# Performance work log

Hardware: AMD Instinct MI355X
Metric: run time of the kernel (lower is better)

Reference implementation:

```python
import jax, jax.numpy as jnp
import numpy as np

K = 3  # filter_size
PAD = (K - 1) // 2


def setup_inputs() -> dict:
    key = jax.random.key(0)
    k1, k2, k3 = jax.random.split(key, 3)
    B, C, H, Wd = 4, 256, 128, 128
    x = jax.random.normal(k1, (B, C, H, Wd), dtype=jnp.float32)
    # 1x1 conv params: out_channels = C * K^2
    W = jax.random.normal(k2, (C * K * K, C), dtype=jnp.float32) * (1.0 / np.sqrt(C))
    b = jax.random.normal(k3, (C * K * K,), dtype=jnp.float32) * 0.01
    return {"x": x, "W": W, "b": b}


def _extract_patches(x):
    # x: (B,C,H,W) -> (B,C,H,W,K*K), kernel positions row-major (matches F.unfold)
    B, C, H, Wd = x.shape
    xp = jnp.pad(x, ((0, 0), (0, 0), (PAD, PAD), (PAD, PAD)))
    patches = jnp.stack(
        [xp[:, :, i:i + H, j:j + Wd] for i in range(K) for j in range(K)],
        axis=-1,
    )
    return patches


def reference(x, W, b):
    B, C, H, Wd = x.shape
    # 1x1 conv: (B,C,H,W) x (C*K^2, C) -> (B, C*K^2, H, W)
    filters = jnp.einsum('bchw,oc->bohw', x, W) + b[None, :, None, None]
    # view(B, C, K^2, H, W) then permute to (B,C,H,W,K^2)
    filters = filters.reshape(B, C, K * K, H, Wd).transpose(0, 1, 3, 4, 2)
    patches = _extract_patches(x)  # (B,C,H,W,K^2), unfold ordering c-major then pos
    return jnp.sum(patches * filters, axis=-1)  # (B,C,H,W)
```

## Files before the change

### kernel.cpp

```cpp
#include <hip/hip_runtime.h>


typedef __attribute__((ext_vector_type(8))) short bf16x8;
typedef __attribute__((ext_vector_type(4))) float f32x4;

__device__ __forceinline__ unsigned int f2bf(float f) {
    unsigned int u = __float_as_uint(f);
    return (u + 0x7fffu + ((u >> 16) & 1u)) >> 16;
}
__device__ __forceinline__ unsigned int pack2(float a, float b) {
    return f2bf(a) | (f2bf(b) << 16);
}

__global__ __launch_bounds__(256) void wconv_kernel(const float* __restrict__ W,
                                                    unsigned char* __restrict__ Wb) {
    int idx0 = blockIdx.x * 256 + threadIdx.x;
    int o = idx0 >> 5, g = idx0 & 31;
    const float4* src = (const float4*)(W + ((size_t)o << 8) + ((size_t)g << 3));
    float4 v0 = src[0], v1 = src[1];
    uint4 pk;
    pk.x = pack2(v0.x, v0.y); pk.y = pack2(v0.z, v0.w);
    pk.z = pack2(v1.x, v1.y); pk.w = pack2(v1.z, v1.w);
    int kh = g >> 4, g2 = g & 15, s = g2 >> 2, kq = g2 & 3;
    int chunk = o / 144, oc = o - chunk * 144;
    int c_local = oc / 9, p = oc - c_local * 9;
    int q = c_local >> 2, c4 = c_local & 3;
    int idx = c4 * 9 + p;
    int ni = idx >> 2, j = idx & 3, r = (q << 2) + j;
    int jsub = kh * 3 + ni / 3, ni_ = ni % 3;
    size_t dst = (size_t)chunk * 73728 + (size_t)jsub * 12288
               + (size_t)(s * 3 + ni_) * 1024 + (size_t)((kq << 4) + r) * 16;
    *(uint4*)(Wb + dst) = pk;
}


#define SYNC_VM(N) asm volatile("s_waitcnt vmcnt(" #N ") lgkmcnt(0)\n\ts_barrier" ::: "memory")
#define SYNC_LG    asm volatile("s_waitcnt lgkmcnt(0)\n\ts_barrier" ::: "memory")
#define FENCE      asm volatile("" ::: "memory")

#define STAGE(CH, J)                                                            \
    do {                                                                        \
        const unsigned char* bs_ = Wb + (size_t)(CH) * 73728                    \
            + (size_t)(J) * 12288 + wv * 3072 + (lane << 4);                    \
        unsigned char* bd_ = smem + (size_t)(J) * 12288 + wv * 3072;            \
        _Pragma("unroll")                                                       \
        for (int c_ = 0; c_ < 3; ++c_)                                          \
            __builtin_amdgcn_global_load_lds(                                   \
                (const __attribute__((address_space(1))) void*)(bs_ + c_ * 1024), \
                (__attribute__((address_space(3))) void*)(bd_ + c_ * 1024), 16, 0, 0); \
    } while (0)

#define MFMA_SUB(J)                                                             \
    do {                                                                        \
        const int kh_ = (J) / 3, snib_ = ((J) % 3) * 3;                         \
        const unsigned char* bb_ = smem + (size_t)(J) * 12288 + (lane << 4);    \
        _Pragma("unroll")                                                       \
        for (int s_ = 0; s_ < 4; ++s_) {                                        \
            const bf16x8 a0_ = afr[(kh_ << 2) + s_];                            \
            const bf16x8 a1_ = afr[8 + (kh_ << 2) + s_];                        \
            _Pragma("unroll")                                                   \
            for (int ni_ = 0; ni_ < 3; ++ni_) {                                 \
                const bf16x8 bq_ = *(const bf16x8*)(bb_ + ((s_ * 3 + ni_) << 10)); \
                acc[0][snib_ + ni_] = __builtin_amdgcn_mfma_f32_16x16x32_bf16(  \
                    bq_, a0_, acc[0][snib_ + ni_], 0, 0, 0);                    \
                acc[1][snib_ + ni_] = __builtin_amdgcn_mfma_f32_16x16x32_bf16(  \
                    bq_, a1_, acc[1][snib_ + ni_], 0, 0, 0);                    \
            }                                                                   \
        }                                                                       \
    } while (0)

__global__ __launch_bounds__(256, 2) void dfgemm_kernel(
        const unsigned char* __restrict__ Wb, const float* __restrict__ x,
        const float* __restrict__ bias, float* __restrict__ out) {
    __shared__ __align__(16) unsigned char smem[73728];

    const int t = threadIdx.x;
    const int lane = t & 63, wv = t >> 6;
    const int quad = lane >> 4, lrow = lane & 15;

    const int b = blockIdx.x >> 7;
    const int h = blockIdx.x & 127;

    STAGE(0, 0); STAGE(0, 1); STAGE(0, 2);
    STAGE(0, 3); STAGE(0, 4); STAGE(0, 5);

    bf16x8 afr[16];
    {
        const float* xrow = x + ((size_t)b << 22) + (h << 7);
        #pragma unroll
        for (int mi = 0; mi < 2; ++mi) {
            const int w = (wv << 5) + (mi << 4) + lrow;
            #pragma unroll
            for (int gg = 0; gg < 8; ++gg) {
                const float* p = xrow + ((size_t)((gg << 5) + (quad << 3)) << 14) + w;
                float v[8];
                #pragma unroll
                for (int e = 0; e < 8; ++e) v[e] = p[(size_t)e << 14];
                uint4 pk;
                pk.x = pack2(v[0], v[1]); pk.y = pack2(v[2], v[3]);
                pk.z = pack2(v[4], v[5]); pk.w = pack2(v[6], v[7]);
                afr[(mi << 3) + gg] = *(const bf16x8*)&pk;
            }
        }
    }
    SYNC_VM(0);

    #pragma unroll 1
    for (int chunk = 0; chunk < 16; ++chunk) {
        const int c1 = (chunk + 1) & 15;
        f32x4 acc[2][9];
        const f32x4 zero = {0.f, 0.f, 0.f, 0.f};
        #pragma unroll
        for (int mi = 0; mi < 2; ++mi)
            #pragma unroll
            for (int ni = 0; ni < 9; ++ni) acc[mi][ni] = zero;

        SYNC_VM(8);

        MFMA_SUB(0); MFMA_SUB(1); MFMA_SUB(2);
        MFMA_SUB(3); MFMA_SUB(4); MFMA_SUB(5);

        SYNC_LG;

        STAGE(c1, 0); STAGE(c1, 1); STAGE(c1, 2);
        STAGE(c1, 3); STAGE(c1, 4); STAGE(c1, 5);
        FENCE;

        #pragma unroll
        for (int mi = 0; mi < 2; ++mi) {
            const int w = (wv << 5) + (mi << 4) + lrow;
            #pragma unroll
            for (int c4 = 0; c4 < 4; ++c4) {
                const int cg = (chunk << 4) + (quad << 2) + c4;
                const float* bp = bias + cg * 9;
                const float* xc = x + ((size_t)((b << 8) + cg) << 14);
                float sum = 0.f;
                #pragma unroll
                for (int p = 0; p < 9; ++p) {
                    const int idx = c4 * 9 + p;
                    const int ni = idx >> 2, j = idx & 3;
                    const float yv = acc[mi][ni][j];
                    const int hh = h + p / 3 - 1, ww = w + p % 3 - 1;
                    float xv = 0.f;
                    if ((unsigned)hh < 128u && (unsigned)ww < 128u)
                        xv = xc[(hh << 7) + ww];
                    sum += (yv + bp[p]) * xv;
                }
                out[((size_t)((b << 8) + cg) << 14) + (h << 7) + w] = sum;
            }
        }
    }
}

extern "C" void kernel_launch(void* const* d_in, const int* in_sizes, int n_in,
                              void* d_out, int out_size, void* d_ws, size_t ws_size,
                              hipStream_t stream) {
    const float* x    = (const float*)d_in[0];
    const float* W    = (const float*)d_in[1];
    const float* bias = (const float*)d_in[2];
    float* out = (float*)d_out;

    unsigned char* Wb = (unsigned char*)d_ws;

    wconv_kernel<<<288, 256, 0, stream>>>(W, Wb);
    dfgemm_kernel<<<512, 256, 0, stream>>>(Wb, x, bias, out);
}
```

Measured before the change: 204.1 us.

## Split channel chunks across two blocks and ring-buffer weight staging in LDS

Each row is now handled by two blocks that each process half of the 16 channel chunks, which doubles the grid. Weight staging moves from a full 72KB chunk buffer to a 4-slot 48KB ring, and the next sub-tile loads are interleaved with the MFMA on the current one using finer vmcnt waits. The smaller LDS footprint allows 3 blocks per CU. The trade-off is that every block re-reads and re-converts the full input row fragment, so x loads double, and there are more barriers per chunk.

```diff
diff --git a/kernel.cpp b/kernel.cpp
--- a/kernel.cpp
+++ b/kernel.cpp
@@ -35,14 +35,13 @@
 
 
 #define SYNC_VM(N) asm volatile("s_waitcnt vmcnt(" #N ") lgkmcnt(0)\n\ts_barrier" ::: "memory")
-#define SYNC_LG    asm volatile("s_waitcnt lgkmcnt(0)\n\ts_barrier" ::: "memory")
 #define FENCE      asm volatile("" ::: "memory")
 
-#define STAGE(CH, J)                                                            \
+#define STAGE(CH, J, BUF)                                                       \
     do {                                                                        \
         const unsigned char* bs_ = Wb + (size_t)(CH) * 73728                    \
             + (size_t)(J) * 12288 + wv * 3072 + (lane << 4);                    \
-        unsigned char* bd_ = smem + (size_t)(J) * 12288 + wv * 3072;            \
+        unsigned char* bd_ = smem + (size_t)(BUF) * 12288 + wv * 3072;          \
         _Pragma("unroll")                                                       \
         for (int c_ = 0; c_ < 3; ++c_)                                          \
             __builtin_amdgcn_global_load_lds(                                   \
@@ -50,10 +49,10 @@
                 (__attribute__((address_space(3))) void*)(bd_ + c_ * 1024), 16, 0, 0); \
     } while (0)
 
-#define MFMA_SUB(J)                                                             \
+#define MFMA_SUB(J, BUF)                                                        \
     do {                                                                        \
         const int kh_ = (J) / 3, snib_ = ((J) % 3) * 3;                         \
-        const unsigned char* bb_ = smem + (size_t)(J) * 12288 + (lane << 4);    \
+        const unsigned char* bb_ = smem + (size_t)(BUF) * 12288 + (lane << 4);  \
         _Pragma("unroll")                                                       \
         for (int s_ = 0; s_ < 4; ++s_) {                                        \
             const bf16x8 a0_ = afr[(kh_ << 2) + s_];                            \
@@ -69,20 +68,22 @@
         }                                                                       \
     } while (0)
 
-__global__ __launch_bounds__(256, 2) void dfgemm_kernel(
+__global__ __launch_bounds__(256, 3) void dfgemm_kernel(
         const unsigned char* __restrict__ Wb, const float* __restrict__ x,
         const float* __restrict__ bias, float* __restrict__ out) {
-    __shared__ __align__(16) unsigned char smem[73728];
+    __shared__ __align__(16) unsigned char smem[49152];
 
     const int t = threadIdx.x;
     const int lane = t & 63, wv = t >> 6;
     const int quad = lane >> 4, lrow = lane & 15;
 
-    const int b = blockIdx.x >> 7;
-    const int h = blockIdx.x & 127;
+    const int half = blockIdx.x & 1;
+    const int rowid = blockIdx.x >> 1;
+    const int b = rowid >> 7;
+    const int h = rowid & 127;
+    const int c0 = half << 3;
 
-    STAGE(0, 0); STAGE(0, 1); STAGE(0, 2);
-    STAGE(0, 3); STAGE(0, 4); STAGE(0, 5);
+    STAGE(c0, 0, 0); STAGE(c0, 1, 1); STAGE(c0, 2, 2);
 
     bf16x8 afr[16];
     {
@@ -106,8 +107,10 @@
     SYNC_VM(0);
 
     #pragma unroll 1
-    for (int chunk = 0; chunk < 16; ++chunk) {
-        const int c1 = (chunk + 1) & 15;
+    for (int lc = 0; lc < 8; ++lc) {
+        const int chunk = c0 + lc;
+        const int cnext = c0 + ((lc + 1) & 7);
+        const int bb0 = (lc * 6) & 3;
         f32x4 acc[2][9];
         const f32x4 zero = {0.f, 0.f, 0.f, 0.f};
         #pragma unroll
@@ -116,14 +119,28 @@
             for (int ni = 0; ni < 9; ++ni) acc[mi][ni] = zero;
 
         SYNC_VM(8);
+        STAGE(chunk, 3, (bb0 + 3) & 3);
+        MFMA_SUB(0, bb0);
 
-        MFMA_SUB(0); MFMA_SUB(1); MFMA_SUB(2);
-        MFMA_SUB(3); MFMA_SUB(4); MFMA_SUB(5);
+        SYNC_VM(11);
+        STAGE(chunk, 4, (bb0 + 4) & 3);
+        MFMA_SUB(1, (bb0 + 1) & 3);
 
-        SYNC_LG;
+        SYNC_VM(14);
+        STAGE(chunk, 5, (bb0 + 5) & 3);
+        MFMA_SUB(2, (bb0 + 2) & 3);
 
-        STAGE(c1, 0); STAGE(c1, 1); STAGE(c1, 2);
-        STAGE(c1, 3); STAGE(c1, 4); STAGE(c1, 5);
+        SYNC_VM(6);
+        STAGE(cnext, 0, (bb0 + 6) & 3);
+        MFMA_SUB(3, (bb0 + 3) & 3);
+
+        SYNC_VM(6);
+        STAGE(cnext, 1, (bb0 + 7) & 3);
+        MFMA_SUB(4, (bb0 + 4) & 3);
+
+        SYNC_VM(6);
+        STAGE(cnext, 2, (bb0 + 8) & 3);
+        MFMA_SUB(5, (bb0 + 5) & 3);
         FENCE;
 
         #pragma unroll
@@ -163,5 +180,5 @@
     unsigned char* Wb = (unsigned char*)d_ws;
 
     wconv_kernel<<<288, 256, 0, stream>>>(W, Wb);
-    dfgemm_kernel<<<512, 256, 0, stream>>>(Wb, x, bias, out);
+    dfgemm_kernel<<<1024, 256, 0, stream>>>(Wb, x, bias, out);
 }
```

New measurement: 311.1 us. 52.4% more time.
